# Kernel optimization log

Measured on AMD Instinct MI355X. Metric: run time of the kernel, lower is better.

## Reference

```python
import jax, jax.numpy as jnp
import numpy as np

B, N, H = 4, 256, 512
P = 128  # game_physics_params


def _init(key, shape, scale=0.02):
    return jax.random.normal(key, shape, dtype=jnp.float32) * scale


def setup_inputs() -> dict:
    key = jax.random.key(0)
    ks = jax.random.split(key, 16)
    return {
        "object_features": jax.random.normal(ks[0], (B, N, H), dtype=jnp.float32),
        # physics_predictor: H -> 512 -> P
        "pp_w1": _init(ks[1], (H, 512)), "pp_b1": jnp.zeros((512,), jnp.float32),
        "pp_w2": _init(ks[2], (512, P)), "pp_b2": jnp.zeros((P,), jnp.float32),
        # collision_detector: 2H -> 256 -> 128 -> 1
        "cd_w1": _init(ks[3], (2 * H, 256)), "cd_b1": jnp.zeros((256,), jnp.float32),
        "cd_w2": _init(ks[4], (256, 128)), "cd_b2": jnp.zeros((128,), jnp.float32),
        "cd_w3": _init(ks[5], (128, 1)), "cd_b3": jnp.zeros((1,), jnp.float32),
        # velocity / force heads: H -> 3
        "vel_w": _init(ks[6], (H, 3)), "vel_b": jnp.zeros((3,), jnp.float32),
        "frc_w": _init(ks[7], (H, 3)), "frc_b": jnp.zeros((3,), jnp.float32),
    }


def reference(object_features, pp_w1, pp_b1, pp_w2, pp_b2,
              cd_w1, cd_b1, cd_w2, cd_b2, cd_w3, cd_b3,
              vel_w, vel_b, frc_w, frc_b):
    x = object_features  # [B, N, H]
    # physics predictor MLP
    p = jax.nn.relu(x @ pp_w1 + pp_b1) @ pp_w2 + pp_b2  # [B, N, P]
    mass = jax.nn.sigmoid(p[..., 0:1]) * 100.0
    friction = jax.nn.sigmoid(p[..., 1:2])
    elasticity = jax.nn.sigmoid(p[..., 2:3])
    density = jax.nn.sigmoid(p[..., 3:4]) * 10.0
    velocities = x @ vel_w + vel_b  # [B, N, 3]
    forces = x @ frc_w + frc_b      # [B, N, 3]

    # vectorized pairwise collision detection over upper-triangle pairs
    iu, ju = np.triu_indices(N, k=1)  # static index arrays, length Np = N(N-1)/2
    pairs = jnp.concatenate([x[:, iu], x[:, ju]], axis=-1)  # [B, Np, 2H]
    h = jax.nn.relu(pairs @ cd_w1 + cd_b1)
    h = jax.nn.relu(h @ cd_w2 + cd_b2)
    prob = jax.nn.sigmoid(h @ cd_w3 + cd_b3)[..., 0]  # [B, Np]
    collision_matrix = jnp.zeros((x.shape[0], N, N), dtype=x.dtype)
    collision_matrix = collision_matrix.at[:, iu, ju].set(prob).at[:, ju, iu].set(prob)

    return (mass, friction, elasticity, density, velocities, forces, collision_matrix)
```

## Files before the change

### kernel.cpp

```cpp
#include <hip/hip_runtime.h>
#include <hip/hip_bf16.h>

typedef __attribute__((ext_vector_type(8))) short bf16x8;
typedef __attribute__((ext_vector_type(4))) float f32x4;

__device__ __forceinline__ float sigmoidf_(float v) {
    return 1.0f / (1.0f + __expf(-v));
}
__device__ __forceinline__ short f2bf(float f) {
    union { __hip_bfloat16 h; short s; } cv;
    cv.h = __float2bfloat16(f);
    return cv.s;
}
__device__ __forceinline__ float bf2f(short s) {
    union { float f; unsigned u; } cv;
    cv.u = ((unsigned)(unsigned short)s) << 16;
    return cv.f;
}

__global__ __launch_bounds__(256) void convert_kernel(
    const float* __restrict__ x, const float* __restrict__ pp_w1,
    const float* __restrict__ cd_w1, const float* __restrict__ cd_w2,
    const float* __restrict__ pp_w2, const float* __restrict__ vel_w,
    const float* __restrict__ frc_w,
    __hip_bfloat16* __restrict__ xb, __hip_bfloat16* __restrict__ Wt,
    __hip_bfloat16* __restrict__ w2t, float* __restrict__ hw)
{
    __shared__ float ts[64][65];
    const int b = blockIdx.x, t = threadIdx.x;

    if (b < 256) {
        int base = b * 2048 + t * 8;
        float4 a = *(const float4*)(x + base);
        float4 c = *(const float4*)(x + base + 4);
        bf16x8 o;
        o[0] = f2bf(a.x); o[1] = f2bf(a.y); o[2] = f2bf(a.z); o[3] = f2bf(a.w);
        o[4] = f2bf(c.x); o[5] = f2bf(c.y); o[6] = f2bf(c.z); o[7] = f2bf(c.w);
        *(bf16x8*)(xb + base) = o;
        return;
    }
    if (b == 392) {
        for (int e = t; e < 5120; e += 256) {
            int h = e >> 9, k = e & 511;
            float v = (h < 4) ? pp_w2[k * 128 + h]
                    : (h < 7) ? vel_w[k * 3 + (h - 4)]
                              : frc_w[k * 3 + (h - 7)];
            hw[e] = v;
        }
        return;
    }

    const float* src; int ss, k0, n0, region;
    if (b < 320)      { int i = b - 256; src = pp_w1; ss = 512; k0 = (i >> 3) * 64; n0 = (i & 7) * 64; region = 0; }
    else if (b < 384) { int i = b - 320; src = cd_w1; ss = 256; k0 = (i >> 2) * 64; n0 = (i & 3) * 64; region = 1; }
    else              { int i = b - 384; src = cd_w2; ss = 128; k0 = (i >> 1) * 64; n0 = (i & 1) * 64; region = 2; }

    #pragma unroll
    for (int i = 0; i < 4; ++i) {
        int r = (t >> 4) + i * 16, c4 = (t & 15) * 4;
        *(float4*)&ts[r][c4] = *(const float4*)(src + (k0 + r) * ss + n0 + c4);
    }
    __syncthreads();
    #pragma unroll
    for (int i = 0; i < 4; ++i) {
        int nOut = (t >> 4) + i * 16, kc = (t & 15) * 4;
        ushort4 o;
        o.x = (unsigned short)f2bf(ts[kc + 0][nOut]);
        o.y = (unsigned short)f2bf(ts[kc + 1][nOut]);
        o.z = (unsigned short)f2bf(ts[kc + 2][nOut]);
        o.w = (unsigned short)f2bf(ts[kc + 3][nOut]);
        int gn = n0 + nOut, gk = k0 + kc;
        if (region == 0)      *(ushort4*)(Wt + gn * 512 + gk) = o;
        else if (region == 1) {
            int row = (gk < 512) ? (512 + gn) : (768 + gn);
            *(ushort4*)(Wt + row * 512 + (gk & 511)) = o;
        } else                *(ushort4*)(w2t + gn * 256 + gk) = o;
    }
}

__global__ __launch_bounds__(256) void gemm_kernel(
    const __hip_bfloat16* __restrict__ xb, const __hip_bfloat16* __restrict__ Wt,
    const float* __restrict__ pp_b1, const float* __restrict__ cd_b1,
    __hip_bfloat16* __restrict__ hidg, float* __restrict__ Ug,
    float* __restrict__ Vg)
{
    const int t = threadIdx.x;
    const int wave = t >> 6, lane = t & 63;
    const int l = lane & 15, q = lane >> 4;
    const int m0 = blockIdx.y * 32;
    const int n0 = blockIdx.x * 128 + wave * 32;

    const __hip_bfloat16* a0p = xb + (m0 + l) * 512 + q * 8;
    const __hip_bfloat16* a1p = a0p + 16 * 512;
    const __hip_bfloat16* b0p = Wt + (n0 + l) * 512 + q * 8;
    const __hip_bfloat16* b1p = b0p + 16 * 512;

    f32x4 acc00 = {}, acc01 = {}, acc10 = {}, acc11 = {};
    #pragma unroll
    for (int ks = 0; ks < 16; ++ks) {
        bf16x8 a0 = *(const bf16x8*)(a0p + ks * 32);
        bf16x8 a1 = *(const bf16x8*)(a1p + ks * 32);
        bf16x8 b0 = *(const bf16x8*)(b0p + ks * 32);
        bf16x8 b1 = *(const bf16x8*)(b1p + ks * 32);
        acc00 = __builtin_amdgcn_mfma_f32_16x16x32_bf16(a0, b0, acc00, 0, 0, 0);
        acc01 = __builtin_amdgcn_mfma_f32_16x16x32_bf16(a0, b1, acc01, 0, 0, 0);
        acc10 = __builtin_amdgcn_mfma_f32_16x16x32_bf16(a1, b0, acc10, 0, 0, 0);
        acc11 = __builtin_amdgcn_mfma_f32_16x16x32_bf16(a1, b1, acc11, 0, 0, 0);
    }

    const int c0 = n0 + l, c1 = n0 + 16 + l;
    #pragma unroll
    for (int mt = 0; mt < 2; ++mt) {
        const f32x4& A0 = mt ? acc10 : acc00;
        const f32x4& A1 = mt ? acc11 : acc01;
        if (n0 < 512) {
            float b0v = pp_b1[c0], b1v = pp_b1[c1];
            #pragma unroll
            for (int r = 0; r < 4; ++r) {
                int rg = m0 + mt * 16 + q * 4 + r;
                hidg[rg * 512 + c0] = __float2bfloat16(fmaxf(A0[r] + b0v, 0.f));
                hidg[rg * 512 + c1] = __float2bfloat16(fmaxf(A1[r] + b1v, 0.f));
            }
        } else if (n0 < 768) {
            float b0v = cd_b1[c0 - 512], b1v = cd_b1[c1 - 512];
            #pragma unroll
            for (int r = 0; r < 4; ++r) {
                int rg = m0 + mt * 16 + q * 4 + r;
                Ug[rg * 256 + (c0 - 512)] = A0[r] + b0v;
                Ug[rg * 256 + (c1 - 512)] = A1[r] + b1v;
            }
        } else {
            #pragma unroll
            for (int r = 0; r < 4; ++r) {
                int rg = m0 + mt * 16 + q * 4 + r;
                Vg[rg * 256 + (c0 - 768)] = A0[r] + 0.f;
                Vg[rg * 256 + (c1 - 768)] = A1[r] + 0.f;
            }
        }
    }
}

__global__ __launch_bounds__(256) void pair_kernel(
    const float* __restrict__ Ug, const float* __restrict__ Vg,
    const __hip_bfloat16* __restrict__ w2t,
    const float* __restrict__ cd_b2, const float* __restrict__ cd_w3,
    const float* __restrict__ cd_b3, float* __restrict__ cm,
    const float* __restrict__ x, const __hip_bfloat16* __restrict__ hidg,
    const float* __restrict__ hw, const float* __restrict__ pp_b2,
    const float* __restrict__ vel_b, const float* __restrict__ frc_b,
    float* __restrict__ out)
{
    __shared__ __align__(16) __hip_bfloat16 hs[16384];
    __shared__ float ps[64][4];

    const int t = threadIdx.x;
    const int wave = t >> 6, lane = t & 63;

    if (blockIdx.x >= 528) {
        const int row = blockIdx.y * 256 + (blockIdx.x - 528) * 4 + wave;
        const float4* xr = (const float4*)(x + row * 512);
        float4 xa = xr[lane * 2], xc = xr[lane * 2 + 1];
        bf16x8 hb = *(const bf16x8*)(hidg + row * 512 + lane * 8);
        float hf[8];
        #pragma unroll
        for (int j = 0; j < 8; ++j) hf[j] = bf2f(hb[j]);

        #pragma unroll
        for (int h = 0; h < 10; ++h) {
            const float4* wr = (const float4*)(hw + h * 512);
            float4 wa = wr[lane * 2], wc = wr[lane * 2 + 1];
            float s;
            if (h < 4) {
                s = hf[0]*wa.x + hf[1]*wa.y + hf[2]*wa.z + hf[3]*wa.w
                  + hf[4]*wc.x + hf[5]*wc.y + hf[6]*wc.z + hf[7]*wc.w;
            } else {
                s = xa.x*wa.x + xa.y*wa.y + xa.z*wa.z + xa.w*wa.w
                  + xc.x*wc.x + xc.y*wc.y + xc.z*wc.z + xc.w*wc.w;
            }
            s += __shfl_xor(s, 1);  s += __shfl_xor(s, 2);
            s += __shfl_xor(s, 4);  s += __shfl_xor(s, 8);
            s += __shfl_xor(s, 16); s += __shfl_xor(s, 32);
            if (lane == 0) {
                if (h < 4) {
                    float sg = sigmoidf_(s + pp_b2[h]);
                    out[h * 1024 + row] = (h == 0) ? sg * 100.f : (h == 3) ? sg * 10.f : sg;
                } else if (h < 7) {
                    out[4096 + row * 3 + (h - 4)] = s + vel_b[h - 4];
                } else {
                    out[7168 + row * 3 + (h - 7)] = s + frc_b[h - 7];
                }
            }
        }
        return;
    }

    const int b = blockIdx.y;
    const int tp = blockIdx.x;
    int ti = (int)((65.0f - sqrtf(4225.0f - 8.0f * (float)tp)) * 0.5f);
    while ((ti + 1) * (65 - (ti + 1)) / 2 <= tp) ++ti;
    while (ti * (65 - ti) / 2 > tp) --ti;
    const int tj = ti + (tp - ti * (65 - ti) / 2);

    const int i0 = ti * 8, j0 = tj * 8;

    {
        const float* Ub = Ug + (b * 256 + i0) * 256;
        const float* Vb = Vg + (b * 256 + j0) * 256;
        #pragma unroll
        for (int w = 0; w < 8; ++w) {
            int idx = (w << 8) + t;
            int p = idx >> 5, c = idx & 31;
            const float* up = Ub + (p >> 3) * 256 + c * 8;
            const float* vp = Vb + (p & 7) * 256 + c * 8;
            float4 u0 = *(const float4*)up, u1 = *(const float4*)(up + 4);
            float4 v0 = *(const float4*)vp, v1 = *(const float4*)(vp + 4);
            bf16x8 o;
            o[0] = f2bf(fmaxf(u0.x + v0.x, 0.f));
            o[1] = f2bf(fmaxf(u0.y + v0.y, 0.f));
            o[2] = f2bf(fmaxf(u0.z + v0.z, 0.f));
            o[3] = f2bf(fmaxf(u0.w + v0.w, 0.f));
            o[4] = f2bf(fmaxf(u1.x + v1.x, 0.f));
            o[5] = f2bf(fmaxf(u1.y + v1.y, 0.f));
            o[6] = f2bf(fmaxf(u1.z + v1.z, 0.f));
            o[7] = f2bf(fmaxf(u1.w + v1.w, 0.f));
            int byte = (p << 9) + (c << 4);
            byte ^= (p & 7) << 4;
            *(bf16x8*)((char*)hs + byte) = o;
        }
    }
    __syncthreads();

    const int l = lane & 15, q = lane >> 4;
    const __hip_bfloat16* wb0 = w2t + ((wave * 2 + 0) * 16 + l) * 256 + q * 8;
    const __hip_bfloat16* wb1 = wb0 + 16 * 256;
    const char* hsb = (const char*)hs;
    const int xorv = (l & 7) << 4;
    const int rbase = (l << 9) + (q << 4);

    f32x4 acc[4][2] = {};
    #pragma unroll
    for (int ks = 0; ks < 8; ++ks) {
        bf16x8 bfr0 = *(const bf16x8*)(wb0 + ks * 32);
        bf16x8 bfr1 = *(const bf16x8*)(wb1 + ks * 32);
        #pragma unroll
        for (int mt = 0; mt < 4; ++mt) {
            int byte = (mt << 13) + rbase + (ks << 6);
            bf16x8 afr = *(const bf16x8*)(hsb + (byte ^ xorv));
            acc[mt][0] = __builtin_amdgcn_mfma_f32_16x16x32_bf16(afr, bfr0, acc[mt][0], 0, 0, 0);
            acc[mt][1] = __builtin_amdgcn_mfma_f32_16x16x32_bf16(afr, bfr1, acc[mt][1], 0, 0, 0);
        }
    }

    float b2v0 = cd_b2[(wave * 2 + 0) * 16 + l], b2v1 = cd_b2[(wave * 2 + 1) * 16 + l];
    float w3v0 = cd_w3[(wave * 2 + 0) * 16 + l], w3v1 = cd_w3[(wave * 2 + 1) * 16 + l];
    #pragma unroll
    for (int mt = 0; mt < 4; ++mt) {
        #pragma unroll
        for (int r = 0; r < 4; ++r) {
            float g0 = fmaxf(acc[mt][0][r] + b2v0, 0.f);
            float g1 = fmaxf(acc[mt][1][r] + b2v1, 0.f);
            float s = g0 * w3v0 + g1 * w3v1;
            s += __shfl_xor(s, 1);
            s += __shfl_xor(s, 2);
            s += __shfl_xor(s, 4);
            s += __shfl_xor(s, 8);
            if (l == 0) ps[mt * 16 + q * 4 + r][wave] = s;
        }
    }
    __syncthreads();

    if (t < 64) {
        int p = t;
        float v = ps[p][0] + ps[p][1] + ps[p][2] + ps[p][3] + cd_b3[0];
        float prob = 1.0f / (1.0f + __expf(-v));
        int i = i0 + (p >> 3), j = j0 + (p & 7);
        float* base = cm + b * 65536;
        if (i < j) {
            base[i * 256 + j] = prob;
            base[j * 256 + i] = prob;
        } else if (i == j) {
            base[i * 256 + i] = 0.0f;
        }
    }
}

extern "C" void kernel_launch(void* const* d_in, const int* in_sizes, int n_in,
                              void* d_out, int out_size, void* d_ws, size_t ws_size,
                              hipStream_t stream) {
    const float* x     = (const float*)d_in[0];
    const float* pp_w1 = (const float*)d_in[1];
    const float* pp_b1 = (const float*)d_in[2];
    const float* pp_w2 = (const float*)d_in[3];
    const float* pp_b2 = (const float*)d_in[4];
    const float* cd_w1 = (const float*)d_in[5];
    const float* cd_b1 = (const float*)d_in[6];
    const float* cd_w2 = (const float*)d_in[7];
    const float* cd_b2 = (const float*)d_in[8];
    const float* cd_w3 = (const float*)d_in[9];
    const float* cd_b3 = (const float*)d_in[10];
    const float* vel_w = (const float*)d_in[11];
    const float* vel_b = (const float*)d_in[12];
    const float* frc_w = (const float*)d_in[13];
    const float* frc_b = (const float*)d_in[14];

    float* out = (float*)d_out;
    float* Ug = (float*)d_ws;
    float* Vg = Ug + 262144;
    __hip_bfloat16* xb   = (__hip_bfloat16*)(Vg + 262144);
    __hip_bfloat16* Wt   = xb + 524288;
    __hip_bfloat16* hidg = Wt + 524288;
    __hip_bfloat16* w2t  = hidg + 524288;
    float* hw = (float*)(w2t + 32768);

    convert_kernel<<<dim3(393), dim3(256), 0, stream>>>(
        x, pp_w1, cd_w1, cd_w2, pp_w2, vel_w, frc_w, xb, Wt, w2t, hw);
    gemm_kernel<<<dim3(8, 32), dim3(256), 0, stream>>>(
        xb, Wt, pp_b1, cd_b1, hidg, Ug, Vg);
    pair_kernel<<<dim3(592, 4), dim3(256), 0, stream>>>(
        Ug, Vg, w2t, cd_b2, cd_w3, cd_b3, out + 10240,
        x, hidg, hw, pp_b2, vel_b, frc_b, out);
}
```

Measured before the change: 136.0 us.

## Software-pipeline pair kernel over batches with double-buffered half-K LDS tiles

The pair kernel now processes all four batches inside one block instead of one batch per blockIdx.y. The 256-wide hidden dimension is split into two halves, and each half is staged through a double-buffered LDS tile, so the global loads for the next stage are issued before the MFMAs on the current stage. The grid shrinks from 592x4 to 656 blocks, and each head block now handles eight rows instead of four. The aim is to hide U/V load latency and cut per-block setup cost, at the price of more registers for the prefetch buffers and fewer resident blocks.

```diff
diff --git a/kernel.cpp b/kernel.cpp
--- a/kernel.cpp
+++ b/kernel.cpp
@@ -133,8 +133,8 @@
             #pragma unroll
             for (int r = 0; r < 4; ++r) {
                 int rg = m0 + mt * 16 + q * 4 + r;
-                Vg[rg * 256 + (c0 - 768)] = A0[r] + 0.f;
-                Vg[rg * 256 + (c1 - 768)] = A1[r] + 0.f;
+                Vg[rg * 256 + (c0 - 768)] = A0[r];
+                Vg[rg * 256 + (c1 - 768)] = A1[r];
             }
         }
     }
@@ -150,138 +150,177 @@
     const float* __restrict__ vel_b, const float* __restrict__ frc_b,
     float* __restrict__ out)
 {
-    __shared__ __align__(16) __hip_bfloat16 hs[16384];
-    __shared__ float ps[64][4];
+    __shared__ __align__(16) __hip_bfloat16 hsH[2][8192];
+    __shared__ float ps[2][64][4];
 
     const int t = threadIdx.x;
     const int wave = t >> 6, lane = t & 63;
-
-    if (blockIdx.x >= 528) {
-        const int row = blockIdx.y * 256 + (blockIdx.x - 528) * 4 + wave;
-        const float4* xr = (const float4*)(x + row * 512);
-        float4 xa = xr[lane * 2], xc = xr[lane * 2 + 1];
-        bf16x8 hb = *(const bf16x8*)(hidg + row * 512 + lane * 8);
-        float hf[8];
-        #pragma unroll
-        for (int j = 0; j < 8; ++j) hf[j] = bf2f(hb[j]);
-
-        #pragma unroll
-        for (int h = 0; h < 10; ++h) {
-            const float4* wr = (const float4*)(hw + h * 512);
-            float4 wa = wr[lane * 2], wc = wr[lane * 2 + 1];
-            float s;
-            if (h < 4) {
-                s = hf[0]*wa.x + hf[1]*wa.y + hf[2]*wa.z + hf[3]*wa.w
-                  + hf[4]*wc.x + hf[5]*wc.y + hf[6]*wc.z + hf[7]*wc.w;
-            } else {
-                s = xa.x*wa.x + xa.y*wa.y + xa.z*wa.z + xa.w*wa.w
-                  + xc.x*wc.x + xc.y*wc.y + xc.z*wc.z + xc.w*wc.w;
-            }
-            s += __shfl_xor(s, 1);  s += __shfl_xor(s, 2);
-            s += __shfl_xor(s, 4);  s += __shfl_xor(s, 8);
-            s += __shfl_xor(s, 16); s += __shfl_xor(s, 32);
-            if (lane == 0) {
+    const int bx = blockIdx.x;
+
+    if (bx >= 528) {
+        #pragma unroll
+        for (int rr = 0; rr < 2; ++rr) {
+            const int row = (bx - 528) * 8 + wave * 2 + rr;
+            const float4* xr = (const float4*)(x + row * 512);
+            float4 xa = xr[lane * 2], xc = xr[lane * 2 + 1];
+            bf16x8 hb = *(const bf16x8*)(hidg + row * 512 + lane * 8);
+            float hf[8];
+            #pragma unroll
+            for (int j = 0; j < 8; ++j) hf[j] = bf2f(hb[j]);
+
+            #pragma unroll
+            for (int h = 0; h < 10; ++h) {
+                const float4* wr = (const float4*)(hw + h * 512);
+                float4 wa = wr[lane * 2], wc = wr[lane * 2 + 1];
+                float s;
                 if (h < 4) {
-                    float sg = sigmoidf_(s + pp_b2[h]);
-                    out[h * 1024 + row] = (h == 0) ? sg * 100.f : (h == 3) ? sg * 10.f : sg;
-                } else if (h < 7) {
-                    out[4096 + row * 3 + (h - 4)] = s + vel_b[h - 4];
+                    s = hf[0]*wa.x + hf[1]*wa.y + hf[2]*wa.z + hf[3]*wa.w
+                      + hf[4]*wc.x + hf[5]*wc.y + hf[6]*wc.z + hf[7]*wc.w;
                 } else {
-                    out[7168 + row * 3 + (h - 7)] = s + frc_b[h - 7];
+                    s = xa.x*wa.x + xa.y*wa.y + xa.z*wa.z + xa.w*wa.w
+                      + xc.x*wc.x + xc.y*wc.y + xc.z*wc.z + xc.w*wc.w;
                 }
+                s += __shfl_xor(s, 1);  s += __shfl_xor(s, 2);
+                s += __shfl_xor(s, 4);  s += __shfl_xor(s, 8);
+                s += __shfl_xor(s, 16); s += __shfl_xor(s, 32);
+                if (lane == 0) {
+                    if (h < 4) {
+                        float sg = sigmoidf_(s + pp_b2[h]);
+                        out[h * 1024 + row] = (h == 0) ? sg * 100.f : (h == 3) ? sg * 10.f : sg;
+                    } else if (h < 7) {
+                        out[4096 + row * 3 + (h - 4)] = s + vel_b[h - 4];
+                    } else {
+                        out[7168 + row * 3 + (h - 7)] = s + frc_b[h - 7];
+                    }
+                }
             }
         }
         return;
     }
 
-    const int b = blockIdx.y;
-    const int tp = blockIdx.x;
+    const int tp = bx;
     int ti = (int)((65.0f - sqrtf(4225.0f - 8.0f * (float)tp)) * 0.5f);
     while ((ti + 1) * (65 - (ti + 1)) / 2 <= tp) ++ti;
     while (ti * (65 - ti) / 2 > tp) --ti;
     const int tj = ti + (tp - ti * (65 - ti) / 2);
-
     const int i0 = ti * 8, j0 = tj * 8;
 
-    {
-        const float* Ub = Ug + (b * 256 + i0) * 256;
-        const float* Vb = Vg + (b * 256 + j0) * 256;
-        #pragma unroll
-        for (int w = 0; w < 8; ++w) {
+    const int l = lane & 15, q = lane >> 4;
+    const int xorv = (l & 7) << 4;
+
+    const __hip_bfloat16* wb0 = w2t + ((wave * 2 + 0) * 16 + l) * 256 + q * 8;
+    const __hip_bfloat16* wb1 = wb0 + 16 * 256;
+    const float b2v0 = cd_b2[(wave * 2 + 0) * 16 + l];
+    const float b2v1 = cd_b2[(wave * 2 + 1) * 16 + l];
+    const float w3v0 = cd_w3[(wave * 2 + 0) * 16 + l];
+    const float w3v1 = cd_w3[(wave * 2 + 1) * 16 + l];
+    const float b3 = cd_b3[0];
+
+    f32x4 acc[4][2];
+    float4 ru0[4], ru1[4], rv0[4], rv1[4];
+
+    auto ISSUE = [&](int u, int h) {
+        const float* Ub = Ug + ((u << 8) + i0) * 256 + (h << 7);
+        const float* Vb = Vg + ((u << 8) + j0) * 256 + (h << 7);
+        #pragma unroll
+        for (int w = 0; w < 4; ++w) {
             int idx = (w << 8) + t;
-            int p = idx >> 5, c = idx & 31;
+            int p = idx >> 4, c = idx & 15;
             const float* up = Ub + (p >> 3) * 256 + c * 8;
             const float* vp = Vb + (p & 7) * 256 + c * 8;
-            float4 u0 = *(const float4*)up, u1 = *(const float4*)(up + 4);
-            float4 v0 = *(const float4*)vp, v1 = *(const float4*)(vp + 4);
+            ru0[w] = *(const float4*)up;  ru1[w] = *(const float4*)(up + 4);
+            rv0[w] = *(const float4*)vp;  rv1[w] = *(const float4*)(vp + 4);
+        }
+    };
+    auto WRITE = [&](int buf) {
+        char* dst = (char*)hsH[buf];
+        #pragma unroll
+        for (int w = 0; w < 4; ++w) {
+            int idx = (w << 8) + t;
+            int p = idx >> 4, c = idx & 15;
             bf16x8 o;
-            o[0] = f2bf(fmaxf(u0.x + v0.x, 0.f));
-            o[1] = f2bf(fmaxf(u0.y + v0.y, 0.f));
-            o[2] = f2bf(fmaxf(u0.z + v0.z, 0.f));
-            o[3] = f2bf(fmaxf(u0.w + v0.w, 0.f));
-            o[4] = f2bf(fmaxf(u1.x + v1.x, 0.f));
-            o[5] = f2bf(fmaxf(u1.y + v1.y, 0.f));
-            o[6] = f2bf(fmaxf(u1.z + v1.z, 0.f));
-            o[7] = f2bf(fmaxf(u1.w + v1.w, 0.f));
-            int byte = (p << 9) + (c << 4);
-            byte ^= (p & 7) << 4;
-            *(bf16x8*)((char*)hs + byte) = o;
-        }
-    }
+            o[0] = f2bf(fmaxf(ru0[w].x + rv0[w].x, 0.f));
+            o[1] = f2bf(fmaxf(ru0[w].y + rv0[w].y, 0.f));
+            o[2] = f2bf(fmaxf(ru0[w].z + rv0[w].z, 0.f));
+            o[3] = f2bf(fmaxf(ru0[w].w + rv0[w].w, 0.f));
+            o[4] = f2bf(fmaxf(ru1[w].x + rv1[w].x, 0.f));
+            o[5] = f2bf(fmaxf(ru1[w].y + rv1[w].y, 0.f));
+            o[6] = f2bf(fmaxf(ru1[w].z + rv1[w].z, 0.f));
+            o[7] = f2bf(fmaxf(ru1[w].w + rv1[w].w, 0.f));
+            int byte = (p << 8) + (((c << 4)) ^ ((p & 7) << 4));
+            *(bf16x8*)(dst + byte) = o;
+        }
+    };
+    auto MFMAH = [&](int h, int buf) {
+        const char* src = (const char*)hsH[buf];
+        #pragma unroll
+        for (int ks = 0; ks < 4; ++ks) {
+            bf16x8 bfr0 = *(const bf16x8*)(wb0 + (h * 4 + ks) * 32);
+            bf16x8 bfr1 = *(const bf16x8*)(wb1 + (h * 4 + ks) * 32);
+            #pragma unroll
+            for (int mt = 0; mt < 4; ++mt) {
+                int byte = (mt << 12) + (l << 8) + (((ks << 6) + (q << 4)) ^ xorv);
+                bf16x8 afr = *(const bf16x8*)(src + byte);
+                acc[mt][0] = __builtin_amdgcn_mfma_f32_16x16x32_bf16(afr, bfr0, acc[mt][0], 0, 0, 0);
+                acc[mt][1] = __builtin_amdgcn_mfma_f32_16x16x32_bf16(afr, bfr1, acc[mt][1], 0, 0, 0);
+            }
+        }
+    };
+    auto EPI = [&](int u) {
+        #pragma unroll
+        for (int mt = 0; mt < 4; ++mt) {
+            #pragma unroll
+            for (int r = 0; r < 4; ++r) {
+                float g0 = fmaxf(acc[mt][0][r] + b2v0, 0.f);
+                float g1 = fmaxf(acc[mt][1][r] + b2v1, 0.f);
+                float s = g0 * w3v0 + g1 * w3v1;
+                s += __shfl_xor(s, 1);
+                s += __shfl_xor(s, 2);
+                s += __shfl_xor(s, 4);
+                s += __shfl_xor(s, 8);
+                if (l == 0) ps[u & 1][mt * 16 + q * 4 + r][wave] = s;
+            }
+        }
+    };
+    auto FIN = [&](int u) {
+        if (t < 64) {
+            int p = t;
+            float v = ps[u & 1][p][0] + ps[u & 1][p][1] + ps[u & 1][p][2]
+                    + ps[u & 1][p][3] + b3;
+            float prob = 1.0f / (1.0f + __expf(-v));
+            int i = i0 + (p >> 3), j = j0 + (p & 7);
+            float* base = cm + u * 65536;
+            if (i < j) {
+                base[i * 256 + j] = prob;
+                base[j * 256 + i] = prob;
+            } else if (i == j) {
+                base[i * 256 + i] = 0.0f;
+            }
+        }
+    };
+
+    ISSUE(0, 0);
+    WRITE(0);
     __syncthreads();
 
-    const int l = lane & 15, q = lane >> 4;
-    const __hip_bfloat16* wb0 = w2t + ((wave * 2 + 0) * 16 + l) * 256 + q * 8;
-    const __hip_bfloat16* wb1 = wb0 + 16 * 256;
-    const char* hsb = (const char*)hs;
-    const int xorv = (l & 7) << 4;
-    const int rbase = (l << 9) + (q << 4);
-
-    f32x4 acc[4][2] = {};
-    #pragma unroll
-    for (int ks = 0; ks < 8; ++ks) {
-        bf16x8 bfr0 = *(const bf16x8*)(wb0 + ks * 32);
-        bf16x8 bfr1 = *(const bf16x8*)(wb1 + ks * 32);
-        #pragma unroll
-        for (int mt = 0; mt < 4; ++mt) {
-            int byte = (mt << 13) + rbase + (ks << 6);
-            bf16x8 afr = *(const bf16x8*)(hsb + (byte ^ xorv));
-            acc[mt][0] = __builtin_amdgcn_mfma_f32_16x16x32_bf16(afr, bfr0, acc[mt][0], 0, 0, 0);
-            acc[mt][1] = __builtin_amdgcn_mfma_f32_16x16x32_bf16(afr, bfr1, acc[mt][1], 0, 0, 0);
-        }
-    }
-
-    float b2v0 = cd_b2[(wave * 2 + 0) * 16 + l], b2v1 = cd_b2[(wave * 2 + 1) * 16 + l];
-    float w3v0 = cd_w3[(wave * 2 + 0) * 16 + l], w3v1 = cd_w3[(wave * 2 + 1) * 16 + l];
-    #pragma unroll
-    for (int mt = 0; mt < 4; ++mt) {
-        #pragma unroll
-        for (int r = 0; r < 4; ++r) {
-            float g0 = fmaxf(acc[mt][0][r] + b2v0, 0.f);
-            float g1 = fmaxf(acc[mt][1][r] + b2v1, 0.f);
-            float s = g0 * w3v0 + g1 * w3v1;
-            s += __shfl_xor(s, 1);
-            s += __shfl_xor(s, 2);
-            s += __shfl_xor(s, 4);
-            s += __shfl_xor(s, 8);
-            if (l == 0) ps[mt * 16 + q * 4 + r][wave] = s;
-        }
-    }
-    __syncthreads();
-
-    if (t < 64) {
-        int p = t;
-        float v = ps[p][0] + ps[p][1] + ps[p][2] + ps[p][3] + cd_b3[0];
-        float prob = 1.0f / (1.0f + __expf(-v));
-        int i = i0 + (p >> 3), j = j0 + (p & 7);
-        float* base = cm + b * 65536;
-        if (i < j) {
-            base[i * 256 + j] = prob;
-            base[j * 256 + i] = prob;
-        } else if (i == j) {
-            base[i * 256 + i] = 0.0f;
-        }
-    }
+    #pragma unroll
+    for (int s = 1; s <= 8; ++s) {
+        if (s < 8) ISSUE(s >> 1, s & 1);
+        const int sp = s - 1, u = sp >> 1, h = sp & 1;
+        if (h == 0) {
+            #pragma unroll
+            for (int mt = 0; mt < 4; ++mt) {
+                acc[mt][0] = (f32x4){0.f, 0.f, 0.f, 0.f};
+                acc[mt][1] = (f32x4){0.f, 0.f, 0.f, 0.f};
+            }
+        }
+        MFMAH(h, h);
+        if (h == 1) EPI(u);
+        if ((s & 1) && s >= 3) FIN((s - 3) >> 1);
+        if (s < 8) WRITE(s & 1);
+        __syncthreads();
+    }
+    FIN(3);
 }
 
 extern "C" void kernel_launch(void* const* d_in, const int* in_sizes, int n_in,
@@ -316,7 +355,7 @@
         x, pp_w1, cd_w1, cd_w2, pp_w2, vel_w, frc_w, xb, Wt, w2t, hw);
     gemm_kernel<<<dim3(8, 32), dim3(256), 0, stream>>>(
         xb, Wt, pp_b1, cd_b1, hidg, Ug, Vg);
-    pair_kernel<<<dim3(592, 4), dim3(256), 0, stream>>>(
+    pair_kernel<<<dim3(656), dim3(256), 0, stream>>>(
         Ug, Vg, w2t, cd_b2, cd_w3, cd_b3, out + 10240,
         x, hidg, hw, pp_b2, vel_b, frc_b, out);
 }
```

New measurement: 134.8 us. Within noise of the previous version (-0.8%).

## Store pair projections in bf16 and restructure pair kernel with async LDS loads

Applied to the files above, without the earlier changes.

The GEMM now writes the U/V collision projections as bf16 instead of fp32, which halves their global footprint. The pair kernel is rebuilt as 128-thread blocks over a flattened (tile, batch) grid. Each block loads its U and V rows straight into padded LDS with global_load_lds, then forms relu(U+V) in registers just before each MFMA instead of building a full hidden tile in LDS. Each wave now covers all 128 output columns, so the per-block shared-memory reduction and second barrier go away. The trade-offs are extra bf16 rounding of U and V before the add and more accumulator registers per wave.

```diff
diff --git a/kernel.cpp b/kernel.cpp
--- a/kernel.cpp
+++ b/kernel.cpp
@@ -81,14 +81,14 @@
 __global__ __launch_bounds__(256) void gemm_kernel(
     const __hip_bfloat16* __restrict__ xb, const __hip_bfloat16* __restrict__ Wt,
     const float* __restrict__ pp_b1, const float* __restrict__ cd_b1,
-    __hip_bfloat16* __restrict__ hidg, float* __restrict__ Ug,
-    float* __restrict__ Vg)
+    __hip_bfloat16* __restrict__ hidg, __hip_bfloat16* __restrict__ Ugb,
+    __hip_bfloat16* __restrict__ Vgb)
 {
     const int t = threadIdx.x;
     const int wave = t >> 6, lane = t & 63;
     const int l = lane & 15, q = lane >> 4;
-    const int m0 = blockIdx.y * 32;
-    const int n0 = blockIdx.x * 128 + wave * 32;
+    const int m0 = blockIdx.x * 32;
+    const int n0 = blockIdx.y * 128 + wave * 32;
 
     const __hip_bfloat16* a0p = xb + (m0 + l) * 512 + q * 8;
     const __hip_bfloat16* a1p = a0p + 16 * 512;
@@ -126,22 +126,22 @@
             #pragma unroll
             for (int r = 0; r < 4; ++r) {
                 int rg = m0 + mt * 16 + q * 4 + r;
-                Ug[rg * 256 + (c0 - 512)] = A0[r] + b0v;
-                Ug[rg * 256 + (c1 - 512)] = A1[r] + b1v;
+                Ugb[rg * 256 + (c0 - 512)] = __float2bfloat16(A0[r] + b0v);
+                Ugb[rg * 256 + (c1 - 512)] = __float2bfloat16(A1[r] + b1v);
             }
         } else {
             #pragma unroll
             for (int r = 0; r < 4; ++r) {
                 int rg = m0 + mt * 16 + q * 4 + r;
-                Vg[rg * 256 + (c0 - 768)] = A0[r] + 0.f;
-                Vg[rg * 256 + (c1 - 768)] = A1[r] + 0.f;
-            }
-        }
-    }
-}
-
-__global__ __launch_bounds__(256) void pair_kernel(
-    const float* __restrict__ Ug, const float* __restrict__ Vg,
+                Vgb[rg * 256 + (c0 - 768)] = __float2bfloat16(A0[r]);
+                Vgb[rg * 256 + (c1 - 768)] = __float2bfloat16(A1[r]);
+            }
+        }
+    }
+}
+
+__global__ __launch_bounds__(128, 3) void pair_kernel(
+    const __hip_bfloat16* __restrict__ Ugb, const __hip_bfloat16* __restrict__ Vgb,
     const __hip_bfloat16* __restrict__ w2t,
     const float* __restrict__ cd_b2, const float* __restrict__ cd_w3,
     const float* __restrict__ cd_b3, float* __restrict__ cm,
@@ -150,136 +150,141 @@
     const float* __restrict__ vel_b, const float* __restrict__ frc_b,
     float* __restrict__ out)
 {
-    __shared__ __align__(16) __hip_bfloat16 hs[16384];
-    __shared__ float ps[64][4];
+    __shared__ __align__(16) char lds[8320];
 
     const int t = threadIdx.x;
     const int wave = t >> 6, lane = t & 63;
-
-    if (blockIdx.x >= 528) {
-        const int row = blockIdx.y * 256 + (blockIdx.x - 528) * 4 + wave;
-        const float4* xr = (const float4*)(x + row * 512);
-        float4 xa = xr[lane * 2], xc = xr[lane * 2 + 1];
-        bf16x8 hb = *(const bf16x8*)(hidg + row * 512 + lane * 8);
-        float hf[8];
-        #pragma unroll
-        for (int j = 0; j < 8; ++j) hf[j] = bf2f(hb[j]);
-
-        #pragma unroll
-        for (int h = 0; h < 10; ++h) {
-            const float4* wr = (const float4*)(hw + h * 512);
-            float4 wa = wr[lane * 2], wc = wr[lane * 2 + 1];
-            float s;
-            if (h < 4) {
-                s = hf[0]*wa.x + hf[1]*wa.y + hf[2]*wa.z + hf[3]*wa.w
-                  + hf[4]*wc.x + hf[5]*wc.y + hf[6]*wc.z + hf[7]*wc.w;
-            } else {
-                s = xa.x*wa.x + xa.y*wa.y + xa.z*wa.z + xa.w*wa.w
-                  + xc.x*wc.x + xc.y*wc.y + xc.z*wc.z + xc.w*wc.w;
-            }
-            s += __shfl_xor(s, 1);  s += __shfl_xor(s, 2);
-            s += __shfl_xor(s, 4);  s += __shfl_xor(s, 8);
-            s += __shfl_xor(s, 16); s += __shfl_xor(s, 32);
-            if (lane == 0) {
+    const int bx = blockIdx.x;
+
+    if (bx >= 2112) {
+        const int row0 = (bx - 2112) * 16 + wave * 8;
+        for (int rr = 0; rr < 8; ++rr) {
+            const int row = row0 + rr;
+            const float4* xr = (const float4*)(x + row * 512);
+            float4 xa = xr[lane * 2], xc = xr[lane * 2 + 1];
+            bf16x8 hb = *(const bf16x8*)(hidg + row * 512 + lane * 8);
+            float hf[8];
+            #pragma unroll
+            for (int j = 0; j < 8; ++j) hf[j] = bf2f(hb[j]);
+
+            #pragma unroll
+            for (int h = 0; h < 10; ++h) {
+                const float4* wr = (const float4*)(hw + h * 512);
+                float4 wa = wr[lane * 2], wc = wr[lane * 2 + 1];
+                float s;
                 if (h < 4) {
-                    float sg = sigmoidf_(s + pp_b2[h]);
-                    out[h * 1024 + row] = (h == 0) ? sg * 100.f : (h == 3) ? sg * 10.f : sg;
-                } else if (h < 7) {
-                    out[4096 + row * 3 + (h - 4)] = s + vel_b[h - 4];
+                    s = hf[0]*wa.x + hf[1]*wa.y + hf[2]*wa.z + hf[3]*wa.w
+                      + hf[4]*wc.x + hf[5]*wc.y + hf[6]*wc.z + hf[7]*wc.w;
                 } else {
-                    out[7168 + row * 3 + (h - 7)] = s + frc_b[h - 7];
+                    s = xa.x*wa.x + xa.y*wa.y + xa.z*wa.z + xa.w*wa.w
+                      + xc.x*wc.x + xc.y*wc.y + xc.z*wc.z + xc.w*wc.w;
                 }
+                s += __shfl_xor(s, 1);  s += __shfl_xor(s, 2);
+                s += __shfl_xor(s, 4);  s += __shfl_xor(s, 8);
+                s += __shfl_xor(s, 16); s += __shfl_xor(s, 32);
+                if (lane == 0) {
+                    if (h < 4) {
+                        float sg = sigmoidf_(s + pp_b2[h]);
+                        out[h * 1024 + row] = (h == 0) ? sg * 100.f : (h == 3) ? sg * 10.f : sg;
+                    } else if (h < 7) {
+                        out[4096 + row * 3 + (h - 4)] = s + vel_b[h - 4];
+                    } else {
+                        out[7168 + row * 3 + (h - 7)] = s + frc_b[h - 7];
+                    }
+                }
             }
         }
         return;
     }
 
-    const int b = blockIdx.y;
-    const int tp = blockIdx.x;
+    const int tp = bx >> 2, u = bx & 3;
     int ti = (int)((65.0f - sqrtf(4225.0f - 8.0f * (float)tp)) * 0.5f);
     while ((ti + 1) * (65 - (ti + 1)) / 2 <= tp) ++ti;
     while (ti * (65 - ti) / 2 > tp) --ti;
     const int tj = ti + (tp - ti * (65 - ti) / 2);
-
     const int i0 = ti * 8, j0 = tj * 8;
 
+    const int l = lane & 15, q = lane >> 4;
+
     {
-        const float* Ub = Ug + (b * 256 + i0) * 256;
-        const float* Vb = Vg + (b * 256 + j0) * 256;
-        #pragma unroll
-        for (int w = 0; w < 8; ++w) {
-            int idx = (w << 8) + t;
-            int p = idx >> 5, c = idx & 31;
-            const float* up = Ub + (p >> 3) * 256 + c * 8;
-            const float* vp = Vb + (p & 7) * 256 + c * 8;
-            float4 u0 = *(const float4*)up, u1 = *(const float4*)(up + 4);
-            float4 v0 = *(const float4*)vp, v1 = *(const float4*)(vp + 4);
-            bf16x8 o;
-            o[0] = f2bf(fmaxf(u0.x + v0.x, 0.f));
-            o[1] = f2bf(fmaxf(u0.y + v0.y, 0.f));
-            o[2] = f2bf(fmaxf(u0.z + v0.z, 0.f));
-            o[3] = f2bf(fmaxf(u0.w + v0.w, 0.f));
-            o[4] = f2bf(fmaxf(u1.x + v1.x, 0.f));
-            o[5] = f2bf(fmaxf(u1.y + v1.y, 0.f));
-            o[6] = f2bf(fmaxf(u1.z + v1.z, 0.f));
-            o[7] = f2bf(fmaxf(u1.w + v1.w, 0.f));
-            int byte = (p << 9) + (c << 4);
-            byte ^= (p & 7) << 4;
-            *(bf16x8*)((char*)hs + byte) = o;
-        }
-    }
+        const __hip_bfloat16* src = (wave == 0)
+            ? (Ugb + ((u << 8) + i0) * 256)
+            : (Vgb + ((u << 8) + j0) * 256);
+        char* dst = lds + wave * 4160;
+        #pragma unroll
+        for (int c = 0; c < 4; ++c) {
+            __builtin_amdgcn_global_load_lds(
+                (const __attribute__((address_space(1))) void*)(src + c * 512),
+                (__attribute__((address_space(3))) void*)(dst + c * 1040), 16, 0, 0);
+        }
+    }
+
+    float b2v[8], w3v[8];
+    #pragma unroll
+    for (int nt = 0; nt < 8; ++nt) {
+        b2v[nt] = cd_b2[nt * 16 + l];
+        w3v[nt] = cd_w3[nt * 16 + l];
+    }
+    const float b3 = cd_b3[0];
+
     __syncthreads();
 
-    const int l = lane & 15, q = lane >> 4;
-    const __hip_bfloat16* wb0 = w2t + ((wave * 2 + 0) * 16 + l) * 256 + q * 8;
-    const __hip_bfloat16* wb1 = wb0 + 16 * 256;
-    const char* hsb = (const char*)hs;
-    const int xorv = (l & 7) << 4;
-    const int rbase = (l << 9) + (q << 4);
-
-    f32x4 acc[4][2] = {};
-    #pragma unroll
+    f32x4 acc[2][8];
+    #pragma unroll
+    for (int mt = 0; mt < 2; ++mt)
+        #pragma unroll
+        for (int nt = 0; nt < 8; ++nt)
+            acc[mt][nt] = (f32x4){0.f, 0.f, 0.f, 0.f};
+
+    const int vrow = l & 7;
+    const char* Vb = lds + 4160 + (vrow >> 1) * 1040 + (vrow & 1) * 512;
+
+    #pragma unroll 2
     for (int ks = 0; ks < 8; ++ks) {
-        bf16x8 bfr0 = *(const bf16x8*)(wb0 + ks * 32);
-        bf16x8 bfr1 = *(const bf16x8*)(wb1 + ks * 32);
-        #pragma unroll
-        for (int mt = 0; mt < 4; ++mt) {
-            int byte = (mt << 13) + rbase + (ks << 6);
-            bf16x8 afr = *(const bf16x8*)(hsb + (byte ^ xorv));
-            acc[mt][0] = __builtin_amdgcn_mfma_f32_16x16x32_bf16(afr, bfr0, acc[mt][0], 0, 0, 0);
-            acc[mt][1] = __builtin_amdgcn_mfma_f32_16x16x32_bf16(afr, bfr1, acc[mt][1], 0, 0, 0);
-        }
-    }
-
-    float b2v0 = cd_b2[(wave * 2 + 0) * 16 + l], b2v1 = cd_b2[(wave * 2 + 1) * 16 + l];
-    float w3v0 = cd_w3[(wave * 2 + 0) * 16 + l], w3v1 = cd_w3[(wave * 2 + 1) * 16 + l];
-    #pragma unroll
-    for (int mt = 0; mt < 4; ++mt) {
+        const int koff = ks * 64 + q * 16;
+        bf16x8 bfr[8];
+        #pragma unroll
+        for (int nt = 0; nt < 8; ++nt)
+            bfr[nt] = *(const bf16x8*)(w2t + (nt * 16 + l) * 256 + ks * 32 + q * 8);
+        #pragma unroll
+        for (int mt = 0; mt < 2; ++mt) {
+            const int urow = (wave << 2) + (mt << 1) + (l >> 3);
+            bf16x8 ub = *(const bf16x8*)(lds + (urow >> 1) * 1040 + (urow & 1) * 512 + koff);
+            bf16x8 vb = *(const bf16x8*)(Vb + koff);
+            bf16x8 afr;
+            #pragma unroll
+            for (int j = 0; j < 8; ++j)
+                afr[j] = f2bf(fmaxf(bf2f(ub[j]) + bf2f(vb[j]), 0.f));
+            #pragma unroll
+            for (int nt = 0; nt < 8; ++nt)
+                acc[mt][nt] = __builtin_amdgcn_mfma_f32_16x16x32_bf16(afr, bfr[nt], acc[mt][nt], 0, 0, 0);
+        }
+    }
+
+    float* base = cm + u * 65536;
+    #pragma unroll
+    for (int mt = 0; mt < 2; ++mt) {
         #pragma unroll
         for (int r = 0; r < 4; ++r) {
-            float g0 = fmaxf(acc[mt][0][r] + b2v0, 0.f);
-            float g1 = fmaxf(acc[mt][1][r] + b2v1, 0.f);
-            float s = g0 * w3v0 + g1 * w3v1;
+            float s = 0.f;
+            #pragma unroll
+            for (int nt = 0; nt < 8; ++nt)
+                s += fmaxf(acc[mt][nt][r] + b2v[nt], 0.f) * w3v[nt];
             s += __shfl_xor(s, 1);
             s += __shfl_xor(s, 2);
             s += __shfl_xor(s, 4);
             s += __shfl_xor(s, 8);
-            if (l == 0) ps[mt * 16 + q * 4 + r][wave] = s;
-        }
-    }
-    __syncthreads();
-
-    if (t < 64) {
-        int p = t;
-        float v = ps[p][0] + ps[p][1] + ps[p][2] + ps[p][3] + cd_b3[0];
-        float prob = 1.0f / (1.0f + __expf(-v));
-        int i = i0 + (p >> 3), j = j0 + (p & 7);
-        float* base = cm + b * 65536;
-        if (i < j) {
-            base[i * 256 + j] = prob;
-            base[j * 256 + i] = prob;
-        } else if (i == j) {
-            base[i * 256 + i] = 0.0f;
+            if (l == 0) {
+                const int p = (wave << 5) + (mt << 4) + (q << 2) + r;
+                const int i = i0 + (p >> 3), j = j0 + (p & 7);
+                float prob = 1.0f / (1.0f + __expf(-(s + b3)));
+                if (i < j) {
+                    base[i * 256 + j] = prob;
+                    base[j * 256 + i] = prob;
+                } else if (i == j) {
+                    base[i * 256 + i] = 0.0f;
+                }
+            }
         }
     }
 }
@@ -304,9 +309,9 @@
     const float* frc_b = (const float*)d_in[14];
 
     float* out = (float*)d_out;
-    float* Ug = (float*)d_ws;
-    float* Vg = Ug + 262144;
-    __hip_bfloat16* xb   = (__hip_bfloat16*)(Vg + 262144);
+    __hip_bfloat16* Ugb  = (__hip_bfloat16*)d_ws;
+    __hip_bfloat16* Vgb  = Ugb + 262144;
+    __hip_bfloat16* xb   = Vgb + 262144;
     __hip_bfloat16* Wt   = xb + 524288;
     __hip_bfloat16* hidg = Wt + 524288;
     __hip_bfloat16* w2t  = hidg + 524288;
@@ -314,9 +319,9 @@
 
     convert_kernel<<<dim3(393), dim3(256), 0, stream>>>(
         x, pp_w1, cd_w1, cd_w2, pp_w2, vel_w, frc_w, xb, Wt, w2t, hw);
-    gemm_kernel<<<dim3(8, 32), dim3(256), 0, stream>>>(
-        xb, Wt, pp_b1, cd_b1, hidg, Ug, Vg);
-    pair_kernel<<<dim3(592, 4), dim3(256), 0, stream>>>(
-        Ug, Vg, w2t, cd_b2, cd_w3, cd_b3, out + 10240,
+    gemm_kernel<<<dim3(32, 8), dim3(256), 0, stream>>>(
+        xb, Wt, pp_b1, cd_b1, hidg, Ugb, Vgb);
+    pair_kernel<<<dim3(2176), dim3(128), 0, stream>>>(
+        Ugb, Vgb, w2t, cd_b2, cd_w3, cd_b3, out + 10240,
         x, hidg, hw, pp_b2, vel_b, frc_b, out);
 }
```

Measured after the change: 149.2 us. 1.1x slower.
